# Performance work log

Measured on AMD Instinct MI355X. Metric: run time of the kernel, lower is better.

Reference implementation:

```python
import jax, jax.numpy as jnp
import numpy as np

DIM, H, HD = 1024, 16, 64
B, S = 2, 2048
LAMBDA_INIT = 0.8


def _mha(x, wq, bq, wk, bk, wv, bv, wo, bo):
    # x: [B,S,DIM]; wq/wk/wv: [DIM,H,HD]; wo: [H,HD,DIM]
    q = jnp.einsum('btd,dhk->bthk', x, wq) + bq
    k = jnp.einsum('bsd,dhk->bshk', x, wk) + bk
    v = jnp.einsum('bsd,dhk->bshk', x, wv) + bv
    scores = jnp.einsum('bthk,bshk->bhts', q, k) / jnp.sqrt(jnp.asarray(HD, x.dtype))
    attn = jax.nn.softmax(scores, axis=-1)
    out = jnp.einsum('bhts,bshk->bthk', attn, v)
    return jnp.einsum('bthk,hkd->btd', out, wo) + bo


def _get_lambda(lambda_param, layer_idx):
    layer_factor = jnp.clip(jnp.asarray(layer_idx, jnp.float32) * 0.3, 0.0, 5.0)
    offset = 0.6 * jnp.exp(-layer_factor)
    lam = jax.nn.sigmoid(lambda_param) * (1.0 - offset) + 0.2
    return jnp.clip(lam, 0.1, 0.9)


def setup_inputs() -> dict:
    key = jax.random.key(0)
    ks = jax.random.split(key, 10)
    sc_in = 1.0 / np.sqrt(DIM)   # fan-in-ish scale for projections
    sc_out = 1.0 / np.sqrt(H * HD)
    d = {
        'x': jax.random.normal(ks[0], (B, S, DIM), jnp.float32),
        'proj_w': jax.random.normal(ks[1], (DIM, DIM), jnp.float32) * sc_in,
        'proj_b': jnp.zeros((DIM,), jnp.float32),
        'lambda_param': jnp.full((1,), np.log(LAMBDA_INIT) - np.log(1.0 - LAMBDA_INIT), jnp.float32),
        'layer_idx': 0,
    }
    for i, kk in zip((1, 2), (ks[2:6], ks[6:10])):
        d[f'wq{i}'] = jax.random.normal(kk[0], (DIM, H, HD), jnp.float32) * sc_in
        d[f'wk{i}'] = jax.random.normal(kk[1], (DIM, H, HD), jnp.float32) * sc_in
        d[f'wv{i}'] = jax.random.normal(kk[2], (DIM, H, HD), jnp.float32) * sc_in
        d[f'wo{i}'] = jax.random.normal(kk[3], (H, HD, DIM), jnp.float32) * sc_out
        d[f'bq{i}'] = jnp.zeros((H, HD), jnp.float32)
        d[f'bk{i}'] = jnp.zeros((H, HD), jnp.float32)
        d[f'bv{i}'] = jnp.zeros((H, HD), jnp.float32)
        d[f'bo{i}'] = jnp.zeros((DIM,), jnp.float32)
    return d


def reference(x, wq1, bq1, wk1, bk1, wv1, bv1, wo1, bo1,
              wq2, bq2, wk2, bk2, wv2, bv2, wo2, bo2,
              proj_w, proj_b, lambda_param, layer_idx):
    out1 = _mha(x, wq1, bq1, wk1, bk1, wv1, bv1, wo1, bo1)
    out2 = _mha(x, wq2, bq2, wk2, bk2, wv2, bv2, wo2, bo2)
    lam = _get_lambda(lambda_param, layer_idx)  # shape (1,)
    y = (1.0 - lam) * out1 + lam * out2
    return jnp.einsum('btd,de->bte', y, proj_w) + proj_b
```

## Files before the change

kernel.cpp:

```cpp
#include <hip/hip_runtime.h>

#define DEVI __device__ __forceinline__

typedef unsigned short u16;
typedef unsigned int u32;
typedef __bf16 bf16x8 __attribute__((ext_vector_type(8)));
typedef float f32x4 __attribute__((ext_vector_type(4)));
typedef float f32x16 __attribute__((ext_vector_type(16)));
typedef int i32x2v __attribute__((ext_vector_type(2)));

#define SCALE_Q 0.1803368801f

typedef const __attribute__((address_space(1))) void cas1_void;
typedef __attribute__((address_space(3))) void as3_void;

DEVI void lds_dma16(const void* g, void* l) {
  __builtin_amdgcn_global_load_lds((cas1_void*)g, (as3_void*)l, 16, 0, 0);
}

DEVI u16 f2bf(float f) {
  union { float f; u32 u; } v; v.f = f;
  u32 r = v.u + 0x7FFFu + ((v.u >> 16) & 1u);
  return (u16)(r >> 16);
}

DEVI float bf2f(u16 v) {
  union { u32 u; float f; } x; x.u = (u32)v << 16; return x.f;
}

DEVI float exp2n(float x) {
#if __has_builtin(__builtin_amdgcn_exp2f)
  return __builtin_amdgcn_exp2f(x);
#else
  return __expf(x * 0.6931471805599453f);
#endif
}

DEVI u32 pk2(float lo, float hi2) {
  union { __bf16 h[2]; u32 u; } p;
  p.h[0] = (__bf16)lo; p.h[1] = (__bf16)hi2;
  return p.u;
}

DEVI void plswap2(u32 a, u32 b, u32& x, u32& y) {
#if __has_builtin(__builtin_amdgcn_permlane32_swap)
  i32x2v r = __builtin_amdgcn_permlane32_swap((int)a, (int)b, false, false);
  x = (u32)r[0]; y = (u32)r[1];
#else
  u32 ta = __shfl_xor(a, 32), tb = __shfl_xor(b, 32);
  const int hi_ = (int)((threadIdx.x & 63) >> 5);
  x = hi_ ? tb : a;
  y = hi_ ? b : ta;
#endif
}

DEVI float lambda_dev(const float* lamp, const int* lidx) {
  float lf = (float)(*lidx) * 0.3f;
  lf = fminf(fmaxf(lf, 0.0f), 5.0f);
  float offset = 0.6f * expf(-lf);
  float s = 1.0f / (1.0f + expf(-lamp[0]));
  float lam = s * (1.0f - offset) + 0.2f;
  return fminf(fmaxf(lam, 0.1f), 0.9f);
}

__global__ __launch_bounds__(256) void k_cvt(const float* __restrict__ x, u16* __restrict__ o) {
  int i = (blockIdx.x * 256 + threadIdx.x) * 8;
  float4 a = *(const float4*)(x + i);
  float4 b = *(const float4*)(x + i + 4);
  union { u16 s[8]; uint4 v; } r;
  r.s[0] = f2bf(a.x); r.s[1] = f2bf(a.y); r.s[2] = f2bf(a.z); r.s[3] = f2bf(a.w);
  r.s[4] = f2bf(b.x); r.s[5] = f2bf(b.y); r.s[6] = f2bf(b.z); r.s[7] = f2bf(b.w);
  *(uint4*)(o + i) = r.v;
}

struct TransArgs {
  const float* src[9];
  u16* dst[9];
  int smode[9];
  int tmode[9];
};

__global__ __launch_bounds__(256) void k_transpose(TransArgs ta, const float* lamp, const int* lidx) {
  __shared__ float tile[32][33];
  int z = blockIdx.z;
  int tx = threadIdx.x & 31, ty = threadIdx.x >> 5;
  int bx = blockIdx.x * 32, by = blockIdx.y * 32;
  const float* s = ta.src[z];
  float sc = 1.0f;
  int m = ta.smode[z];
  if (m == 1) sc = SCALE_Q;
  else if (m >= 2) {
    float lam = lambda_dev(lamp, lidx);
    sc = (m == 2) ? (1.0f - lam) : lam;
  }
  u16* d = ta.dst[z];
  if (ta.tmode[z]) {
#pragma unroll
    for (int i = 0; i < 4; ++i)
      tile[ty + i * 8][tx] = s[(size_t)(by + ty + i * 8) * 1024 + bx + tx];
    __syncthreads();
#pragma unroll
    for (int i = 0; i < 4; ++i) {
      int dr = bx + ty + i * 8;
      d[(size_t)dr * 1024 + by + tx] = f2bf(sc * tile[tx][ty + i * 8]);
    }
  } else {
#pragma unroll
    for (int i = 0; i < 4; ++i) {
      int r = by + ty + i * 8;
      d[(size_t)r * 1024 + bx + tx] = f2bf(sc * s[(size_t)r * 1024 + bx + tx]);
    }
  }
}

__global__ __launch_bounds__(256) void k_bias2(const u16* __restrict__ PWt, const float* __restrict__ bo1,
                                               const float* __restrict__ bo2, const float* __restrict__ pb,
                                               const float* lamp, const int* lidx, float* __restrict__ b2) {
  const float lam = lambda_dev(lamp, lidx);
  const int lane = threadIdx.x & 63;
  const int wv = blockIdx.x * 4 + (threadIdx.x >> 6);
#pragma unroll
  for (int i = 0; i < 4; ++i) {
    const int e = wv * 4 + i;
    const u16* row = PWt + (size_t)e * 1024 + lane * 16;
    float acc = 0.f;
#pragma unroll
    for (int j = 0; j < 16; ++j) {
      const int dd = lane * 16 + j;
      const float bm = (1.0f - lam) * bo1[dd] + lam * bo2[dd];
      acc += bf2f(row[j]) * bm;
    }
    acc += __shfl_xor(acc, 1);  acc += __shfl_xor(acc, 2);
    acc += __shfl_xor(acc, 4);  acc += __shfl_xor(acc, 8);
    acc += __shfl_xor(acc, 16); acc += __shfl_xor(acc, 32);
    if (lane == 0) b2[e] = acc + pb[e];
  }
}

struct GemmArgs {
  const u16* A;
  const u16* Bt;
  const u16* A2;
  const u16* Bt2p;
  const float* bias0[6];
  float bscale[6];
  u16* dstu[6];
  u16* dst3;
  float* dstf;
  int K;
  int mode;
};

__global__ __launch_bounds__(256, 4) void k_gemm(GemmArgs ga) {
  __shared__ __align__(16) u16 smem[16384];
  char* smc = (char*)smem;
  const int t = threadIdx.x;
  const int lane = t & 63;
  const int l15 = lane & 15, hi = lane >> 4;
  const int w = t >> 6, wm = w >> 1, wn = w & 1;
  int m0, n0, z, K, mode = ga.mode;
  const u16* A;
  const u16* Bt;
  if (mode == 0) {
    const int bid = blockIdx.x;
    if (bid >= 1536) {
      mode = 3;
      const int lb = bid - 1536;
      m0 = (lb >> 4) * 128;
      n0 = (lb & 15) * 128;
      z = 0;
      A = ga.A2; Bt = ga.Bt2p; K = 1024;
    } else {
      const int xcd = bid & 7, local = bid >> 3;
      const int nb = xcd * 6 + (local % 6);
      m0 = (local / 6) * 128;
      n0 = nb * 128;
      z = n0 >> 10;
      A = ga.A; Bt = ga.Bt; K = ga.K;
    }
  } else {
    m0 = blockIdx.y * 128; n0 = blockIdx.x * 128; z = 0;
    A = ga.A; Bt = ga.Bt; K = ga.K;
  }

  const char* gA[4];
  const char* gB[4];
  u32 lof[4];
#pragma unroll
  for (int ii = 0; ii < 4; ++ii) {
    int fl = ii * 256 + t;
    int row = fl >> 3;
    int cb = ((fl & 7) * 16) ^ ((row & 7) << 4);
    gA[ii] = (const char*)(A + (size_t)(m0 + row) * K) + cb;
    gB[ii] = (const char*)(Bt + (size_t)(n0 + row) * K) + cb;
    lof[ii] = (u32)(ii * 256 + (t & ~63)) * 16;
  }

  u32 aoff[4], boff[4];
#pragma unroll
  for (int i = 0; i < 4; ++i) {
    int rA = wm * 64 + i * 16 + l15;
    aoff[i] = (u32)rA * 128 + (u32)((hi * 16) ^ ((rA & 7) << 4));
    int rB = wn * 64 + i * 16 + l15;
    boff[i] = 16384u + (u32)rB * 128 + (u32)((hi * 16) ^ ((rB & 7) << 4));
  }

  const f32x4 fz = {0.f, 0.f, 0.f, 0.f};
  f32x4 acc[4][4];
#pragma unroll
  for (int i = 0; i < 4; ++i)
#pragma unroll
    for (int j = 0; j < 4; ++j) acc[i][j] = fz;

  const int NT = K >> 6;
  for (int kt = 0; kt < NT; ++kt) {
    const size_t soff = (size_t)kt * 128;
#pragma unroll
    for (int ii = 0; ii < 4; ++ii) {
      lds_dma16(gA[ii] + soff, smc + lof[ii]);
      lds_dma16(gB[ii] + soff, smc + 16384 + lof[ii]);
    }
    __syncthreads();
#pragma unroll
    for (int kh = 0; kh < 2; ++kh) {
      const u32 kx = (u32)kh << 6;
      bf16x8 af[4], bfr[4];
#pragma unroll
      for (int i = 0; i < 4; ++i) af[i] = *(const bf16x8*)(smc + (aoff[i] ^ kx));
#pragma unroll
      for (int j = 0; j < 4; ++j) bfr[j] = *(const bf16x8*)(smc + (boff[j] ^ kx));
#pragma unroll
      for (int i = 0; i < 4; ++i)
#pragma unroll
        for (int j = 0; j < 4; ++j)
          acc[i][j] = __builtin_amdgcn_mfma_f32_16x16x32_bf16(af[i], bfr[j], acc[i][j], 0, 0, 0);
    }
    __syncthreads();
  }

  const float* b0 = ga.bias0[(mode == 0) ? z : 0];
  const float bsc = (mode == 0) ? ga.bscale[z] : 1.0f;
  const int kind = z % 3;
  u16* du = ga.dstu[z];

#pragma unroll
  for (int i = 0; i < 4; ++i) {
#pragma unroll
    for (int j = 0; j < 4; ++j) {
#pragma unroll
      for (int jj = 0; jj < 4; ++jj) {
        int m = m0 + wm * 64 + i * 16 + hi * 4 + jj;
        int n = n0 + wn * 64 + j * 16 + l15;
        float v = acc[i][j][jj];
        if (mode == 0) {
          int nz = n & 1023;
          v += b0[nz] * bsc;
          int b = m >> 11, s = m & 2047, h = nz >> 6, hd = nz & 63;
          size_t addr;
          if (kind == 0) {
            addr = ((size_t)(b * 16 + h) * 2048 + s) * 64 + hd;
          } else if (kind == 1) {
            int gf = ((s >> 5) * 8 + (hd >> 4) * 2 + ((hd >> 3) & 1)) * 32 + (s & 31);
            addr = ((size_t)(b * 16 + h) * 16384 + gf) * 8 + (hd & 7);
          } else {
            int gf = ((((s >> 6) * 4 + ((s >> 4) & 3)) * 2 + ((s >> 3) & 1)) * 2 + (hd >> 5)) * 32 + (hd & 31);
            addr = ((size_t)(b * 16 + h) * 16384 + gf) * 8 + (s & 7);
          }
          du[addr] = f2bf(v);
        } else if (mode == 3) {
          ga.dst3[(size_t)m * 2048 + n] = f2bf(v);
        } else {
          v += b0[n];
          ga.dstf[(size_t)m * 1024 + n] = v;
        }
      }
    }
  }
}

__global__ __launch_bounds__(256, 2) void k_attn3(const u16* __restrict__ Qg_, const u16* __restrict__ Kg_,
                                                  const u16* __restrict__ Vg_, u16* __restrict__ AO) {
  const int t = threadIdx.x, lane = t & 63, w = t >> 6;
  const int l31 = lane & 31, hi = lane >> 5;
  const int bid = blockIdx.x;
  const int xcd = bid & 7, slot = bid >> 3;
  const int qt = slot & 15;
  const int bhbr = xcd * 8 + (slot >> 4);
  const int br = bhbr >> 5, bh = bhbr & 31;
  const size_t base = ((size_t)br * 32 + bh) * 131072;
  const u16* Qg = Qg_ + base;
  const u16* Kt = Kg_ + base + (size_t)(hi * 256 + l31 * 8);
  const u16* Vt = Vg_ + base + (size_t)(hi * 512 + l31 * 8);
  const int q0 = qt * 128 + w * 32;

  bf16x8 qf[4];
  {
    const u16* qp = Qg + (size_t)(q0 + l31) * 64 + hi * 8;
#pragma unroll
    for (int ks = 0; ks < 4; ++ks) qf[ks] = *(const bf16x8*)(qp + ks * 16);
  }

  f32x16 accO[2];
#pragma unroll
  for (int b = 0; b < 2; ++b)
#pragma unroll
    for (int r = 0; r < 16; ++r) accO[b][r] = 0.f;
  float l_r = 0.f;

  bf16x8 kf[2][4], vf[2][4];
#pragma unroll
  for (int kvs = 0; kvs < 2; ++kvs)
#pragma unroll
    for (int ks = 0; ks < 4; ++ks)
      kf[kvs][ks] = *(const bf16x8*)(Kt + kvs * 2048 + ks * 512);
#pragma unroll
  for (int hs = 0; hs < 2; ++hs)
#pragma unroll
    for (int ks = 0; ks < 4; ++ks)
      vf[hs][ks] = *(const bf16x8*)(Vt + ks * 1024 + hs * 256);

  for (int kvt = 0; kvt < 32; ++kvt) {
    f32x16 st[2];
#pragma unroll
    for (int kvs = 0; kvs < 2; ++kvs)
#pragma unroll
      for (int r = 0; r < 16; ++r) st[kvs][r] = 0.f;
#pragma unroll
    for (int ks = 0; ks < 4; ++ks) {
      st[0] = __builtin_amdgcn_mfma_f32_32x32x16_bf16(kf[0][ks], qf[ks], st[0], 0, 0, 0);
      st[1] = __builtin_amdgcn_mfma_f32_32x32x16_bf16(kf[1][ks], qf[ks], st[1], 0, 0, 0);
    }
    if (kvt < 31) {
      const u16* kp = Kt + (size_t)(kvt + 1) * 4096;
#pragma unroll
      for (int kvs = 0; kvs < 2; ++kvs)
#pragma unroll
        for (int ks = 0; ks < 4; ++ks)
          kf[kvs][ks] = *(const bf16x8*)(kp + kvs * 2048 + ks * 512);
    }

    float sm0 = 0.f, sm1 = 0.f, sm2 = 0.f, sm3 = 0.f;
#pragma unroll
    for (int kvs = 0; kvs < 2; ++kvs)
#pragma unroll
      for (int r = 0; r < 16; r += 4) {
        float p0 = exp2n(st[kvs][r + 0]); st[kvs][r + 0] = p0; sm0 += p0;
        float p1 = exp2n(st[kvs][r + 1]); st[kvs][r + 1] = p1; sm1 += p1;
        float p2 = exp2n(st[kvs][r + 2]); st[kvs][r + 2] = p2; sm2 += p2;
        float p3 = exp2n(st[kvs][r + 3]); st[kvs][r + 3] = p3; sm3 += p3;
      }
    float sum = (sm0 + sm1) + (sm2 + sm3);
    sum += __shfl_xor(sum, 32);
    l_r += sum;

    bf16x8 pa[4];
#pragma unroll
    for (int kvs = 0; kvs < 2; ++kvs)
#pragma unroll
      for (int half = 0; half < 2; ++half) {
        const int rb = half * 8;
        u32 a0 = pk2(st[kvs][rb + 0], st[kvs][rb + 1]);
        u32 a1 = pk2(st[kvs][rb + 2], st[kvs][rb + 3]);
        u32 b0 = pk2(st[kvs][rb + 4], st[kvs][rb + 5]);
        u32 b1 = pk2(st[kvs][rb + 6], st[kvs][rb + 7]);
        u32 w0, w1, w2, w3;
        plswap2(a0, b0, w0, w2);
        plswap2(a1, b1, w1, w3);
        union { u32 u[4]; bf16x8 v; } pk;
        pk.u[0] = w0; pk.u[1] = w1; pk.u[2] = w2; pk.u[3] = w3;
        pa[kvs * 2 + half] = pk.v;
      }

#pragma unroll
    for (int ks = 0; ks < 4; ++ks) {
      accO[0] = __builtin_amdgcn_mfma_f32_32x32x16_bf16(pa[ks], vf[0][ks], accO[0], 0, 0, 0);
      accO[1] = __builtin_amdgcn_mfma_f32_32x32x16_bf16(pa[ks], vf[1][ks], accO[1], 0, 0, 0);
    }
    if (kvt < 31) {
      const u16* vp = Vt + (size_t)(kvt + 1) * 4096;
#pragma unroll
      for (int hs = 0; hs < 2; ++hs)
#pragma unroll
        for (int ks = 0; ks < 4; ++ks)
          vf[hs][ks] = *(const bf16x8*)(vp + ks * 1024 + hs * 256);
    }
  }

  const int b = bh >> 4, h = bh & 15;
  const float inv = 1.0f / l_r;
#pragma unroll
  for (int r = 0; r < 16; ++r) {
    const int qr = (r & 3) + 8 * (r >> 2) + 4 * hi;
    const float iv = __shfl(inv, qr);
    const size_t mrow = (size_t)(b * 2048 + q0 + qr);
#pragma unroll
    for (int hs = 0; hs < 2; ++hs) {
      const int col = br * 1024 + h * 64 + hs * 32 + l31;
      AO[mrow * 2048 + col] = f2bf(accO[hs][r] * iv);
    }
  }
}

extern "C" void kernel_launch(void* const* d_in, const int* in_sizes, int n_in,
                              void* d_out, int out_size, void* d_ws, size_t ws_size,
                              hipStream_t stream) {
  (void)in_sizes; (void)n_in; (void)out_size; (void)ws_size;
  const float* x      = (const float*)d_in[0];
  const float* proj_w = (const float*)d_in[1];
  const float* proj_b = (const float*)d_in[2];
  const float* lamp   = (const float*)d_in[3];
  const int*   lidx   = (const int*)d_in[4];
  const float* wq1 = (const float*)d_in[5];
  const float* wk1 = (const float*)d_in[6];
  const float* wv1 = (const float*)d_in[7];
  const float* wo1 = (const float*)d_in[8];
  const float* bq1 = (const float*)d_in[9];
  const float* bk1 = (const float*)d_in[10];
  const float* bv1 = (const float*)d_in[11];
  const float* bo1 = (const float*)d_in[12];
  const float* wq2 = (const float*)d_in[13];
  const float* wk2 = (const float*)d_in[14];
  const float* wv2 = (const float*)d_in[15];
  const float* wo2 = (const float*)d_in[16];
  const float* bq2 = (const float*)d_in[17];
  const float* bk2 = (const float*)d_in[18];
  const float* bv2 = (const float*)d_in[19];
  const float* bo2 = (const float*)d_in[20];

  char* ws = (char*)d_ws;
  const size_t MB = 1024 * 1024;
  u16* xb   = (u16*)(ws);
  u16* Wt   = (u16*)(ws + 8 * MB);
  u16* WOt2 = (u16*)(ws + 20 * MB);
  u16* PWt  = (u16*)(ws + 24 * MB);
  u16* Qb   = (u16*)(ws + 26 * MB);
  u16* Kb   = (u16*)(ws + 42 * MB);
  u16* Vb   = (u16*)(ws + 58 * MB);
  u16* Bt2  = (u16*)(ws + 74 * MB);
  float* b2 = (float*)(ws + 78 * MB);
  u16* AOb  = (u16*)(ws);

  k_cvt<<<2048, 256, 0, stream>>>(x, xb);

  TransArgs ta;
  const float* srcs[9] = {wq1, wk1, wv1, wq2, wk2, wv2, wo1, wo2, proj_w};
  u16* dsts[9] = {Wt, Wt + 1048576, Wt + 2097152, Wt + 3145728, Wt + 4194304, Wt + 5242880,
                  WOt2, WOt2 + 1048576, PWt};
  int smode[9] = {1, 0, 0, 1, 0, 0, 2, 3, 0};
  int tmode[9] = {1, 1, 1, 1, 1, 1, 0, 0, 1};
  for (int i = 0; i < 9; ++i) {
    ta.src[i] = srcs[i]; ta.dst[i] = dsts[i];
    ta.smode[i] = smode[i]; ta.tmode[i] = tmode[i];
  }
  k_transpose<<<dim3(32, 32, 9), 256, 0, stream>>>(ta, lamp, lidx);

  k_bias2<<<64, 256, 0, stream>>>(PWt, bo1, bo2, proj_b, lamp, lidx, b2);

  GemmArgs g0 = {};
  g0.A = xb; g0.Bt = Wt; g0.K = 1024; g0.mode = 0;
  g0.A2 = PWt; g0.Bt2p = WOt2; g0.dst3 = Bt2;
  const float* qkvb[6] = {bq1, bk1, bv1, bq2, bk2, bv2};
  const size_t BRS = 4194304;
  u16* qkvd[6] = {Qb, Kb, Vb, Qb + BRS, Kb + BRS, Vb + BRS};
  float bsc[6] = {SCALE_Q, 1.f, 1.f, SCALE_Q, 1.f, 1.f};
  for (int i = 0; i < 6; ++i) {
    g0.bias0[i] = qkvb[i];
    g0.bscale[i] = bsc[i];
    g0.dstu[i] = qkvd[i];
  }
  k_gemm<<<dim3(1664), 256, 0, stream>>>(g0);

  k_attn3<<<1024, 256, 0, stream>>>(Qb, Kb, Vb, AOb);

  GemmArgs g2 = {};
  g2.A = AOb; g2.Bt = Bt2; g2.K = 2048; g2.mode = 2;
  g2.bias0[0] = b2;
  g2.dstf = (float*)d_out;
  k_gemm<<<dim3(8, 32), 256, 0, stream>>>(g2);
}
```

Measured before the change: 252.3 us.

## Fold x conversion into transpose launch, raise attention occupancy, use zero-accumulator MFMA

Drops the separate fp32-to-bf16 conversion kernel for x and instead converts x as four extra 1024x1024 slices in the existing batched transpose/convert kernel (non-transposed mode). This saves one kernel launch. The attention kernel's launch bounds go from 2 to 3 blocks per SIMD, which pressures registers and may cause spills. Its first score MFMA now starts from a pinned zero vector instead of re-zeroing the score accumulators every iteration.

Measured after the change: 306.3 us. +21.4%, slower.

```diff
diff --git a/kernel.cpp b/kernel.cpp
--- a/kernel.cpp
+++ b/kernel.cpp
@@ -63,21 +63,11 @@
   return fminf(fmaxf(lam, 0.1f), 0.9f);
 }
 
-__global__ __launch_bounds__(256) void k_cvt(const float* __restrict__ x, u16* __restrict__ o) {
-  int i = (blockIdx.x * 256 + threadIdx.x) * 8;
-  float4 a = *(const float4*)(x + i);
-  float4 b = *(const float4*)(x + i + 4);
-  union { u16 s[8]; uint4 v; } r;
-  r.s[0] = f2bf(a.x); r.s[1] = f2bf(a.y); r.s[2] = f2bf(a.z); r.s[3] = f2bf(a.w);
-  r.s[4] = f2bf(b.x); r.s[5] = f2bf(b.y); r.s[6] = f2bf(b.z); r.s[7] = f2bf(b.w);
-  *(uint4*)(o + i) = r.v;
-}
-
 struct TransArgs {
-  const float* src[9];
-  u16* dst[9];
-  int smode[9];
-  int tmode[9];
+  const float* src[13];
+  u16* dst[13];
+  int smode[13];
+  int tmode[13];
 };
 
 __global__ __launch_bounds__(256) void k_transpose(TransArgs ta, const float* lamp, const int* lidx) {
@@ -278,7 +268,7 @@
   }
 }
 
-__global__ __launch_bounds__(256, 2) void k_attn3(const u16* __restrict__ Qg_, const u16* __restrict__ Kg_,
+__global__ __launch_bounds__(256, 3) void k_attn3(const u16* __restrict__ Qg_, const u16* __restrict__ Kg_,
                                                   const u16* __restrict__ Vg_, u16* __restrict__ AO) {
   const int t = threadIdx.x, lane = t & 63, w = t >> 6;
   const int l31 = lane & 31, hi = lane >> 5;
@@ -301,10 +291,10 @@
   }
 
   f32x16 accO[2];
-#pragma unroll
-  for (int b = 0; b < 2; ++b)
-#pragma unroll
-    for (int r = 0; r < 16; ++r) accO[b][r] = 0.f;
+  f32x16 fz16;
+#pragma unroll
+  for (int r = 0; r < 16; ++r) { accO[0][r] = 0.f; accO[1][r] = 0.f; fz16[r] = 0.f; }
+  asm volatile("" : "+v"(fz16));
   float l_r = 0.f;
 
   bf16x8 kf[2][4], vf[2][4];
@@ -321,12 +311,10 @@
 
   for (int kvt = 0; kvt < 32; ++kvt) {
     f32x16 st[2];
-#pragma unroll
-    for (int kvs = 0; kvs < 2; ++kvs)
-#pragma unroll
-      for (int r = 0; r < 16; ++r) st[kvs][r] = 0.f;
-#pragma unroll
-    for (int ks = 0; ks < 4; ++ks) {
+    st[0] = __builtin_amdgcn_mfma_f32_32x32x16_bf16(kf[0][0], qf[0], fz16, 0, 0, 0);
+    st[1] = __builtin_amdgcn_mfma_f32_32x32x16_bf16(kf[1][0], qf[0], fz16, 0, 0, 0);
+#pragma unroll
+    for (int ks = 1; ks < 4; ++ks) {
       st[0] = __builtin_amdgcn_mfma_f32_32x32x16_bf16(kf[0][ks], qf[ks], st[0], 0, 0, 0);
       st[1] = __builtin_amdgcn_mfma_f32_32x32x16_bf16(kf[1][ks], qf[ks], st[1], 0, 0, 0);
     }
@@ -440,19 +428,19 @@
   float* b2 = (float*)(ws + 78 * MB);
   u16* AOb  = (u16*)(ws);
 
-  k_cvt<<<2048, 256, 0, stream>>>(x, xb);
-
   TransArgs ta;
-  const float* srcs[9] = {wq1, wk1, wv1, wq2, wk2, wv2, wo1, wo2, proj_w};
-  u16* dsts[9] = {Wt, Wt + 1048576, Wt + 2097152, Wt + 3145728, Wt + 4194304, Wt + 5242880,
-                  WOt2, WOt2 + 1048576, PWt};
-  int smode[9] = {1, 0, 0, 1, 0, 0, 2, 3, 0};
-  int tmode[9] = {1, 1, 1, 1, 1, 1, 0, 0, 1};
-  for (int i = 0; i < 9; ++i) {
+  const float* srcs[13] = {wq1, wk1, wv1, wq2, wk2, wv2, wo1, wo2, proj_w,
+                           x, x + 1048576, x + 2097152, x + 3145728};
+  u16* dsts[13] = {Wt, Wt + 1048576, Wt + 2097152, Wt + 3145728, Wt + 4194304, Wt + 5242880,
+                   WOt2, WOt2 + 1048576, PWt,
+                   xb, xb + 1048576, xb + 2097152, xb + 3145728};
+  int smode[13] = {1, 0, 0, 1, 0, 0, 2, 3, 0, 0, 0, 0, 0};
+  int tmode[13] = {1, 1, 1, 1, 1, 1, 0, 0, 1, 0, 0, 0, 0};
+  for (int i = 0; i < 13; ++i) {
     ta.src[i] = srcs[i]; ta.dst[i] = dsts[i];
     ta.smode[i] = smode[i]; ta.tmode[i] = tmode[i];
   }
-  k_transpose<<<dim3(32, 32, 9), 256, 0, stream>>>(ta, lamp, lidx);
+  k_transpose<<<dim3(32, 32, 13), 256, 0, stream>>>(ta, lamp, lidx);
 
   k_bias2<<<64, 256, 0, stream>>>(PWt, bo1, bo2, proj_b, lamp, lidx, b2);
 
```
